# Kernel optimization log

Measured on AMD Instinct MI355X. Metric: run time of the kernel, lower is better.

Reference implementation:

```python
import jax, jax.numpy as jnp
import numpy as np

B, V, H, W = 8, 2, 1024, 1024
N = 131072
TH_MIN, TH_MAX = 0.0, 500.0
ALPHA = 0.5


def _make_extrinsics():
    # Random small-rotation camera-to-world poses (invertible 4x4), fixed seed.
    rng = np.random.default_rng(0)
    E = np.tile(np.eye(4, dtype=np.float32), (B, V, 1, 1))
    for bi in range(B):
        for vi in range(V):
            ang = rng.uniform(-0.15, 0.15)
            ax = rng.normal(size=3)
            ax = ax / np.linalg.norm(ax)
            K = np.array([[0.0, -ax[2], ax[1]], [ax[2], 0.0, -ax[0]], [-ax[1], ax[0], 0.0]])
            R = np.eye(3) + np.sin(ang) * K + (1.0 - np.cos(ang)) * (K @ K)
            E[bi, vi, :3, :3] = R.astype(np.float32)
            E[bi, vi, :3, 3] = (rng.normal(size=3) * 0.5).astype(np.float32)
    return jnp.asarray(E)


def setup_inputs():
    key = jax.random.key(0)
    k0, k1, k2, k3, k4 = jax.random.split(key, 5)
    scale = jnp.array([W - 1.0, H - 1.0], jnp.float32)
    mkpts0 = jax.random.uniform(k0, (N, 2), dtype=jnp.float32) * scale
    mkpts1 = jax.random.uniform(k1, (N, 2), dtype=jnp.float32) * scale
    mconf = jax.random.uniform(k2, (N,), jnp.float32, 0.2, 1.0)
    mbids = jnp.sort(jax.random.randint(k3, (N,), 0, B, dtype=jnp.int32))
    intr = jnp.tile(jnp.array([[1.0, 0.0, 0.5], [0.0, 1.0, 0.5], [0.0, 0.0, 1.0]], jnp.float32), (B, V, 1, 1))
    extr = _make_extrinsics()
    disps = jax.random.uniform(k4, (V * B, 1, H, W), jnp.float32, 0.01, 1.0)
    return {"mkpts0": mkpts0, "mkpts1": mkpts1, "mconf": mconf, "mbids": mbids,
            "intrinsics": intr, "extrinsics": extr, "fullres_disps": disps}


def _forward(mkpts0, mkpts1, mconf, mbids, intrinsics, extrinsics, fullres_disps):
    b, v = intrinsics.shape[:2]
    _, _, h, w = fullres_disps.shape
    # intr0[0,:]*=w ; intr0[1,:]*=h  (normalized -> pixel intrinsics)
    row_scale = jnp.array([float(w), float(h), 1.0], intrinsics.dtype)[None, None, :, None]
    intr = intrinsics * row_scale                                    # (b,v,3,3)
    extr_inv = jnp.linalg.inv(extrinsics)                            # (b,v,4,4)
    proj = jnp.einsum('bvij,bvjk->bvik', intr, extr_inv[:, :, :3, :])  # (b,v,3,4)

    # --- per-keypoint DLT triangulation (vectorized over all N matches) ---
    P = proj[mbids]                                                  # (N,v,3,4)
    pts2 = jnp.stack([mkpts0, mkpts1], axis=1)                       # (N,v,2)
    # rows: conf*(x*P[2]-P[0]), conf*(y*P[2]-P[1])
    A = P[:, :, 2:3, :] * pts2[..., None] - P[:, :, :2, :]           # (N,v,2,4)
    A = A * mconf[:, None, None, None]
    A = A.reshape(-1, 2 * v, 4)                                      # (N,4,4)
    _, _, vh = jnp.linalg.svd(A, full_matrices=False)
    hom = vh[:, -1, :]                                               # last right singular vector
    pts_world = hom[:, :3] / hom[:, 3:4]                             # (N,3)

    # transform into each camera frame: pc_transform(pts, extr.inverse())
    pw_h = jnp.concatenate([pts_world, jnp.ones_like(pts_world[:, :1])], axis=-1)
    pts_cam = jnp.einsum('nvij,nj->nvi', extr_inv[mbids], pw_h)[..., :3]  # (N,v,3)
    z = pts_cam[..., 2]                                              # (N,v)
    valid = jnp.all((z > TH_MIN) & (z < TH_MAX), axis=1)             # (N,)

    # --- near/far over valid matched depths per (scene, view) ---
    zmin = jnp.where(valid[:, None], z, jnp.inf)
    zmax = jnp.where(valid[:, None], z, -jnp.inf)
    near = jax.ops.segment_min(zmin, mbids, num_segments=b)          # (b,v)
    far = jax.ops.segment_max(zmax, mbids, num_segments=b)
    has = jax.ops.segment_max(valid.astype(jnp.float32), mbids, num_segments=b)
    flag = jnp.broadcast_to(has[:, None], (b, v))                    # (b,v)
    near = jnp.where(flag > 0, near, 0.0)
    far = jnp.where(flag > 0, far, 500.0)

    # --- fusion_mkpt_costvolum: scatter 1/z into the cost-volume disparities ---
    disps = fullres_disps.reshape(v, b, h, w)                        # '(v b) 1 h w'
    mk_x = jnp.clip(jnp.stack([mkpts0[:, 0], mkpts1[:, 0]], 1).astype(jnp.int32), 0, w - 1)  # (N,v)
    mk_y = jnp.clip(jnp.stack([mkpts0[:, 1], mkpts1[:, 1]], 1).astype(jnp.int32), 0, h - 1)
    mk_z = 1.0 / z                                                   # matched disparity (N,v)
    view_idx = jnp.broadcast_to(jnp.arange(v, dtype=jnp.int32)[None, :], mk_x.shape)
    bids2 = jnp.broadcast_to(mbids[:, None], mk_x.shape)
    cost = disps[view_idx, bids2, mk_y, mk_x]                        # gather existing disparity
    val = ALPHA * mk_z + (1.0 - ALPHA) * cost                        # alpha-weighted fusion
    val = jnp.where(valid[:, None], val, cost)                       # masked-out matches: no-op write
    disps = disps.at[view_idx, bids2, mk_y, mk_x].set(val)
    fused = disps.reshape(v * b, 1, h, w)
    return fused, near, far, flag


def reference(mkpts0, mkpts1, mconf, mbids, intrinsics, extrinsics, fullres_disps):
    return _forward(mkpts0, mkpts1, mconf, mbids, intrinsics, extrinsics, fullres_disps)
```

## Files before the change

### kernel.cpp

```cpp
#include <hip/hip_runtime.h>
#include <math.h>

#define BB 8
#define VV 2
#define HH 1024
#define WW 1024
#define NPTS 131072
#define IMG (HH*WW)
#define FUSED (VV*BB*IMG)

#define OFF_PD   0u
#define OFF_E2   1536u
#define OFF_HAS  2048u
#define OFF_VAL  2304u
#define OFF_PIX  (2304u + 4u*2u*NPTS)
#define OFF_WIN  (OFF_PIX + 4u*2u*NPTS)
#define WS_NEED  ((size_t)OFF_WIN + 4ull*(size_t)FUSED)

__device__ __forceinline__ int clampi(int v, int lo, int hi) {
    return v < lo ? lo : (v > hi ? hi : v);
}

__global__ __launch_bounds__(64) void prep_kernel(const float* __restrict__ intr,
                            const float* __restrict__ extr,
                            float* __restrict__ out, char* __restrict__ ws) {
    double* Pd  = (double*)(ws + OFF_PD);
    double* e2d = (double*)(ws + OFF_E2);
    int*    hasb = (int*)(ws + OFF_HAS);
    int t = threadIdx.x;
    if (t < BB) hasb[t] = 0;
    if (t < BB * VV) {
        float* near_ = out + FUSED;
        float* far_  = out + FUSED + BB * VV;
        near_[t] = INFINITY;
        far_[t]  = 0.0f;
        const float* E = extr + t * 16;
        double a[4][8];
        for (int i = 0; i < 4; i++)
            for (int j = 0; j < 4; j++) {
                a[i][j]     = (double)E[i * 4 + j];
                a[i][4 + j] = (i == j) ? 1.0 : 0.0;
            }
        for (int c = 0; c < 4; c++) {
            int piv = c; double best = fabs(a[c][c]);
            for (int r = c + 1; r < 4; r++) {
                double v = fabs(a[r][c]);
                if (v > best) { best = v; piv = r; }
            }
            if (piv != c)
                for (int j = 0; j < 8; j++) {
                    double tmp = a[c][j]; a[c][j] = a[piv][j]; a[piv][j] = tmp;
                }
            double inv = 1.0 / a[c][c];
            for (int j = 0; j < 8; j++) a[c][j] *= inv;
            for (int r = 0; r < 4; r++) {
                if (r == c) continue;
                double f = a[r][c];
                for (int j = 0; j < 8; j++) a[r][j] -= f * a[c][j];
            }
        }
        const float* K = intr + t * 9;
        double rs[3] = {(double)WW, (double)HH, 1.0};
        for (int i = 0; i < 3; i++)
            for (int k = 0; k < 4; k++) {
                double s = 0.0;
                for (int j = 0; j < 3; j++) s += (double)K[i * 3 + j] * rs[i] * a[j][4 + k];
                Pd[t * 12 + i * 4 + k] = s;
            }
        for (int k = 0; k < 4; k++) e2d[t * 4 + k] = a[2][4 + k];
    }
}

__global__ __launch_bounds__(256) void copy_kernel(const float4* __restrict__ src,
                                                   float4* __restrict__ dst) {
    int i = blockIdx.x * blockDim.x + threadIdx.x;
    dst[i] = src[i];
}

__global__ __launch_bounds__(256) void clear_kernel(const float* __restrict__ mk0,
                             const float* __restrict__ mk1,
                             const int* __restrict__ mbids, char* __restrict__ ws) {
    int id = blockIdx.x * blockDim.x + threadIdx.x;
    if (id >= 2 * NPTS) return;
    int n = id >> 1, v = id & 1;
    const float* mk = v ? mk1 : mk0;
    int xi = clampi((int)mk[2 * n], 0, WW - 1);
    int yi = clampi((int)mk[2 * n + 1], 0, HH - 1);
    int bid = mbids[n];
    int* winner = (int*)(ws + OFF_WIN);
    winner[(v * BB + bid) * IMG + yi * WW + xi] = -1;
}

template <bool DIRECT>
__global__ __launch_bounds__(256, 2) void solve_kernel(const float* __restrict__ mk0,
                             const float* __restrict__ mk1,
                             const int* __restrict__ mbids, const float* __restrict__ disps,
                             float* __restrict__ out, char* __restrict__ ws) {
    int n = blockIdx.x * blockDim.x + threadIdx.x;
    if (n >= NPTS) return;
    const double* Pd  = (const double*)(ws + OFF_PD);
    const double* e2d = (const double*)(ws + OFF_E2);
    int*   hasb   = (int*)(ws + OFF_HAS);
    float* valarr = (float*)(ws + OFF_VAL);
    int*   pixarr = (int*)(ws + OFF_PIX);
    int*   winner = (int*)(ws + OFF_WIN);
    float* near_  = out + FUSED;
    float* far_   = out + FUSED + BB * VV;

    int bid = mbids[n];
    float xf[2] = {mk0[2 * n], mk1[2 * n]};
    float yf[2] = {mk0[2 * n + 1], mk1[2 * n + 1]};

    double M[4][4];
#pragma unroll
    for (int i = 0; i < 4; i++)
#pragma unroll
        for (int j = 0; j < 4; j++) M[i][j] = 0.0;
#pragma unroll
    for (int v = 0; v < 2; v++) {
        const double* P = Pd + (bid * VV + v) * 12;
        double xx = (double)xf[v], yy = (double)yf[v];
        double r0[4], r1[4];
#pragma unroll
        for (int j = 0; j < 4; j++) {
            r0[j] = xx * P[8 + j] - P[j];
            r1[j] = yy * P[8 + j] - P[4 + j];
        }
#pragma unroll
        for (int i = 0; i < 4; i++)
#pragma unroll
            for (int j = 0; j < 4; j++) M[i][j] += r0[i] * r0[j] + r1[i] * r1[j];
    }

    double Vm[4][4] = {{1, 0, 0, 0}, {0, 1, 0, 0}, {0, 0, 1, 0}, {0, 0, 0, 1}};
    for (int sweep = 0; sweep < 8; ++sweep) {
        double off = fabs(M[0][1]) + fabs(M[0][2]) + fabs(M[0][3]) +
                     fabs(M[1][2]) + fabs(M[1][3]) + fabs(M[2][3]);
        double dia = fabs(M[0][0]) + fabs(M[1][1]) + fabs(M[2][2]) + fabs(M[3][3]);
        if (off <= 1e-13 * dia) break;
#pragma unroll
        for (int p = 0; p < 3; p++) {
#pragma unroll
            for (int q = p + 1; q < 4; q++) {
                double apq = M[p][q];
                if (fabs(apq) < 1e-300) continue;
                double tau = (M[q][q] - M[p][p]) / (2.0 * apq);
                double rt  = sqrt(1.0 + tau * tau);
                double t_  = (tau >= 0.0) ? 1.0 / (tau + rt) : 1.0 / (tau - rt);
                double c = 1.0 / sqrt(1.0 + t_ * t_);
                double s = t_ * c;
#pragma unroll
                for (int k = 0; k < 4; k++) {
                    double mp = M[k][p], mq = M[k][q];
                    M[k][p] = c * mp - s * mq;
                    M[k][q] = s * mp + c * mq;
                }
#pragma unroll
                for (int k = 0; k < 4; k++) {
                    double mp = M[p][k], mq = M[q][k];
                    M[p][k] = c * mp - s * mq;
                    M[q][k] = s * mp + c * mq;
                }
#pragma unroll
                for (int k = 0; k < 4; k++) {
                    double vp = Vm[k][p], vq = Vm[k][q];
                    Vm[k][p] = c * vp - s * vq;
                    Vm[k][q] = s * vp + c * vq;
                }
            }
        }
    }
    int jmin = 0; double dmin = M[0][0];
    if (M[1][1] < dmin) { dmin = M[1][1]; jmin = 1; }
    if (M[2][2] < dmin) { dmin = M[2][2]; jmin = 2; }
    if (M[3][3] < dmin) { dmin = M[3][3]; jmin = 3; }

    double ev[4];
#pragma unroll
    for (int i = 0; i < 4; i++) {
        double a01 = (jmin == 0) ? Vm[i][0] : Vm[i][1];
        double a23 = (jmin == 2) ? Vm[i][2] : Vm[i][3];
        ev[i] = (jmin < 2) ? a01 : a23;
    }

    double iw = 1.0 / ev[3];
    double pwx = ev[0] * iw, pwy = ev[1] * iw, pwz = ev[2] * iw;

    double z[2];
#pragma unroll
    for (int v = 0; v < 2; v++) {
        const double* e = e2d + (bid * VV + v) * 4;
        z[v] = e[0] * pwx + e[1] * pwy + e[2] * pwz + e[3];
    }
    bool valid = (z[0] > 0.0) && (z[0] < 500.0) && (z[1] > 0.0) && (z[1] < 500.0);

    unsigned long long vb = __ballot(valid);
    int bidFirst = __shfl(bid, 0);
    int bidLast  = __shfl(bid, 63);
    if (bidFirst == bidLast) {
        if (vb != 0ULL) {
            float zn[2], zf[2];
#pragma unroll
            for (int v = 0; v < 2; v++) {
                zn[v] = valid ? (float)z[v] : INFINITY;
                zf[v] = valid ? (float)z[v] : -1.0f;
            }
#pragma unroll
            for (int off = 32; off > 0; off >>= 1) {
#pragma unroll
                for (int v = 0; v < 2; v++) {
                    zn[v] = fminf(zn[v], __shfl_down(zn[v], off));
                    zf[v] = fmaxf(zf[v], __shfl_down(zf[v], off));
                }
            }
            if ((threadIdx.x & 63) == 0) {
#pragma unroll
                for (int v = 0; v < 2; v++) {
                    atomicMin((int*)(near_ + bid * VV + v), __float_as_int(zn[v]));
                    atomicMax((int*)(far_  + bid * VV + v), __float_as_int(zf[v]));
                }
                atomicOr(hasb + bid, 1);
            }
        }
    } else if (valid) {
#pragma unroll
        for (int v = 0; v < 2; v++) {
            int fb = __float_as_int((float)z[v]);
            atomicMin((int*)(near_ + bid * VV + v), fb);
            atomicMax((int*)(far_  + bid * VV + v), fb);
        }
        atomicOr(hasb + bid, 1);
    }

#pragma unroll
    for (int v = 0; v < 2; v++) {
        int xi = clampi((int)xf[v], 0, WW - 1);
        int yi = clampi((int)yf[v], 0, HH - 1);
        int pix = (v * BB + bid) * IMG + yi * WW + xi;
        float cost = disps[pix];
        float val = valid ? (float)(0.5 * (1.0 / z[v]) + 0.5 * (double)cost) : cost;
        if (DIRECT) {
            out[pix] = val;
        } else {
            valarr[2 * n + v] = val;
            pixarr[2 * n + v] = pix;
            atomicMax(winner + pix, n);
        }
    }
}

__global__ __launch_bounds__(256) void resolve_kernel(float* __restrict__ out,
                                                      const char* __restrict__ ws) {
    int id = blockIdx.x * blockDim.x + threadIdx.x;
    if (id >= 2 * NPTS) return;
    const float* valarr = (const float*)(ws + OFF_VAL);
    const int*   pixarr = (const int*)(ws + OFF_PIX);
    const int*   winner = (const int*)(ws + OFF_WIN);
    int pix = pixarr[id];
    if (winner[pix] == (id >> 1)) out[pix] = valarr[id];
}

__global__ __launch_bounds__(64) void finalize_kernel(float* __restrict__ out,
                                                      const char* __restrict__ ws) {
    int t = threadIdx.x;
    if (t >= BB * VV) return;
    const int* hasb = (const int*)(ws + OFF_HAS);
    int has = hasb[t / VV];
    float* near_ = out + FUSED;
    float* far_  = out + FUSED + BB * VV;
    float* flag_ = out + FUSED + 2 * BB * VV;
    near_[t] = has ? near_[t] : 0.0f;
    far_[t]  = has ? far_[t]  : 500.0f;
    flag_[t] = has ? 1.0f : 0.0f;
}

extern "C" void kernel_launch(void* const* d_in, const int* in_sizes, int n_in,
                              void* d_out, int out_size, void* d_ws, size_t ws_size,
                              hipStream_t stream) {
    const float* mk0   = (const float*)d_in[0];
    const float* mk1   = (const float*)d_in[1];
    const int*   mbids = (const int*)d_in[3];
    const float* intr  = (const float*)d_in[4];
    const float* extr  = (const float*)d_in[5];
    const float* disps = (const float*)d_in[6];
    float* out = (float*)d_out;
    char*  ws  = (char*)d_ws;

    bool dedup = (ws_size >= WS_NEED);

    prep_kernel<<<1, 64, 0, stream>>>(intr, extr, out, ws);
    copy_kernel<<<FUSED / 4 / 256, 256, 0, stream>>>((const float4*)disps, (float4*)out);
    if (dedup) {
        clear_kernel<<<(2 * NPTS + 255) / 256, 256, 0, stream>>>(mk0, mk1, mbids, ws);
        solve_kernel<false><<<(NPTS + 255) / 256, 256, 0, stream>>>(mk0, mk1, mbids, disps, out, ws);
        resolve_kernel<<<(2 * NPTS + 255) / 256, 256, 0, stream>>>(out, ws);
    } else {
        solve_kernel<true><<<(NPTS + 255) / 256, 256, 0, stream>>>(mk0, mk1, mbids, disps, out, ws);
    }
    finalize_kernel<<<1, 64, 0, stream>>>(out, ws);
}
```

Baseline: 225.9 us.

## Fuse setup kernels, stage projections in LDS, defer disparity gather to resolve

Merges the prep, copy and clear kernels into one launch, and folds finalize into the resolve kernel, cutting the launch count from six to three. The solve kernel now stages the projection and extrinsic rows in shared memory and loads keypoints as float2. It stores z instead of the fused value, so the disparity gather runs only for winning valid matches in resolve. This trades fewer launches and random reads for one more workspace array and branching in the fused kernel.

```diff
diff --git a/kernel.cpp b/kernel.cpp
--- a/kernel.cpp
+++ b/kernel.cpp
@@ -12,104 +12,109 @@
 #define OFF_PD   0u
 #define OFF_E2   1536u
 #define OFF_HAS  2048u
-#define OFF_VAL  2304u
-#define OFF_PIX  (2304u + 4u*2u*NPTS)
-#define OFF_WIN  (OFF_PIX + 4u*2u*NPTS)
+#define OFF_Z    2304u
+#define OFF_PIX  (2304u + 8u*NPTS)
+#define OFF_WIN  (OFF_PIX + 8u*NPTS)
 #define WS_NEED  ((size_t)OFF_WIN + 4ull*(size_t)FUSED)
+
+#define NCOPY  (FUSED/4/256)
+#define NCLEAR ((2*NPTS)/256)
 
 __device__ __forceinline__ int clampi(int v, int lo, int hi) {
     return v < lo ? lo : (v > hi ? hi : v);
 }
 
-__global__ __launch_bounds__(64) void prep_kernel(const float* __restrict__ intr,
-                            const float* __restrict__ extr,
-                            float* __restrict__ out, char* __restrict__ ws) {
-    double* Pd  = (double*)(ws + OFF_PD);
-    double* e2d = (double*)(ws + OFF_E2);
-    int*    hasb = (int*)(ws + OFF_HAS);
+__global__ __launch_bounds__(256) void setup_kernel(
+        const float4* __restrict__ src, float4* __restrict__ dst,
+        const float* __restrict__ mk0, const float* __restrict__ mk1,
+        const int* __restrict__ mbids,
+        const float* __restrict__ intr, const float* __restrict__ extr,
+        float* __restrict__ out, char* __restrict__ ws, int dedup) {
+    int b = blockIdx.x, t = threadIdx.x;
+    if (b < NCOPY) {
+        int i = b * 256 + t;
+        dst[i] = src[i];
+        return;
+    }
+    int cb = b - NCOPY;
+    int id = cb * 256 + t;
+    if (dedup) {
+        int n = id >> 1, v = id & 1;
+        const float* mk = v ? mk1 : mk0;
+        int xi = clampi((int)mk[2 * n], 0, WW - 1);
+        int yi = clampi((int)mk[2 * n + 1], 0, HH - 1);
+        int bid = mbids[n];
+        ((int*)(ws + OFF_WIN))[(v * BB + bid) * IMG + yi * WW + xi] = -1;
+    }
+    if (cb == 0) {
+        if (t < BB) ((int*)(ws + OFF_HAS))[t] = 0;
+        if (t < BB * VV) {
+            float* near_ = out + FUSED;
+            float* far_  = out + FUSED + BB * VV;
+            near_[t] = INFINITY;
+            far_[t]  = 0.0f;
+            double* Pd  = (double*)(ws + OFF_PD);
+            double* e2d = (double*)(ws + OFF_E2);
+            const float* E = extr + t * 16;
+            double a[4][8];
+            for (int i = 0; i < 4; i++)
+                for (int j = 0; j < 4; j++) {
+                    a[i][j]     = (double)E[i * 4 + j];
+                    a[i][4 + j] = (i == j) ? 1.0 : 0.0;
+                }
+            for (int c = 0; c < 4; c++) {
+                int piv = c; double best = fabs(a[c][c]);
+                for (int r = c + 1; r < 4; r++) {
+                    double v = fabs(a[r][c]);
+                    if (v > best) { best = v; piv = r; }
+                }
+                if (piv != c)
+                    for (int j = 0; j < 8; j++) {
+                        double tmp = a[c][j]; a[c][j] = a[piv][j]; a[piv][j] = tmp;
+                    }
+                double inv = 1.0 / a[c][c];
+                for (int j = 0; j < 8; j++) a[c][j] *= inv;
+                for (int r = 0; r < 4; r++) {
+                    if (r == c) continue;
+                    double f = a[r][c];
+                    for (int j = 0; j < 8; j++) a[r][j] -= f * a[c][j];
+                }
+            }
+            const float* K = intr + t * 9;
+            double rs[3] = {(double)WW, (double)HH, 1.0};
+            for (int i = 0; i < 3; i++)
+                for (int k = 0; k < 4; k++) {
+                    double s = 0.0;
+                    for (int j = 0; j < 3; j++) s += (double)K[i * 3 + j] * rs[i] * a[j][4 + k];
+                    Pd[t * 12 + i * 4 + k] = s;
+                }
+            for (int k = 0; k < 4; k++) e2d[t * 4 + k] = a[2][4 + k];
+        }
+    }
+}
+
+template <bool DIRECT>
+__global__ __launch_bounds__(256) void solve_kernel(
+        const float2* __restrict__ mk0, const float2* __restrict__ mk1,
+        const int* __restrict__ mbids, const float* __restrict__ disps,
+        float* __restrict__ out, char* __restrict__ ws) {
+    __shared__ double sD[256];
     int t = threadIdx.x;
-    if (t < BB) hasb[t] = 0;
-    if (t < BB * VV) {
-        float* near_ = out + FUSED;
-        float* far_  = out + FUSED + BB * VV;
-        near_[t] = INFINITY;
-        far_[t]  = 0.0f;
-        const float* E = extr + t * 16;
-        double a[4][8];
-        for (int i = 0; i < 4; i++)
-            for (int j = 0; j < 4; j++) {
-                a[i][j]     = (double)E[i * 4 + j];
-                a[i][4 + j] = (i == j) ? 1.0 : 0.0;
-            }
-        for (int c = 0; c < 4; c++) {
-            int piv = c; double best = fabs(a[c][c]);
-            for (int r = c + 1; r < 4; r++) {
-                double v = fabs(a[r][c]);
-                if (v > best) { best = v; piv = r; }
-            }
-            if (piv != c)
-                for (int j = 0; j < 8; j++) {
-                    double tmp = a[c][j]; a[c][j] = a[piv][j]; a[piv][j] = tmp;
-                }
-            double inv = 1.0 / a[c][c];
-            for (int j = 0; j < 8; j++) a[c][j] *= inv;
-            for (int r = 0; r < 4; r++) {
-                if (r == c) continue;
-                double f = a[r][c];
-                for (int j = 0; j < 8; j++) a[r][j] -= f * a[c][j];
-            }
-        }
-        const float* K = intr + t * 9;
-        double rs[3] = {(double)WW, (double)HH, 1.0};
-        for (int i = 0; i < 3; i++)
-            for (int k = 0; k < 4; k++) {
-                double s = 0.0;
-                for (int j = 0; j < 3; j++) s += (double)K[i * 3 + j] * rs[i] * a[j][4 + k];
-                Pd[t * 12 + i * 4 + k] = s;
-            }
-        for (int k = 0; k < 4; k++) e2d[t * 4 + k] = a[2][4 + k];
-    }
-}
-
-__global__ __launch_bounds__(256) void copy_kernel(const float4* __restrict__ src,
-                                                   float4* __restrict__ dst) {
-    int i = blockIdx.x * blockDim.x + threadIdx.x;
-    dst[i] = src[i];
-}
-
-__global__ __launch_bounds__(256) void clear_kernel(const float* __restrict__ mk0,
-                             const float* __restrict__ mk1,
-                             const int* __restrict__ mbids, char* __restrict__ ws) {
-    int id = blockIdx.x * blockDim.x + threadIdx.x;
-    if (id >= 2 * NPTS) return;
-    int n = id >> 1, v = id & 1;
-    const float* mk = v ? mk1 : mk0;
-    int xi = clampi((int)mk[2 * n], 0, WW - 1);
-    int yi = clampi((int)mk[2 * n + 1], 0, HH - 1);
-    int bid = mbids[n];
-    int* winner = (int*)(ws + OFF_WIN);
-    winner[(v * BB + bid) * IMG + yi * WW + xi] = -1;
-}
-
-template <bool DIRECT>
-__global__ __launch_bounds__(256, 2) void solve_kernel(const float* __restrict__ mk0,
-                             const float* __restrict__ mk1,
-                             const int* __restrict__ mbids, const float* __restrict__ disps,
-                             float* __restrict__ out, char* __restrict__ ws) {
-    int n = blockIdx.x * blockDim.x + threadIdx.x;
-    if (n >= NPTS) return;
-    const double* Pd  = (const double*)(ws + OFF_PD);
-    const double* e2d = (const double*)(ws + OFF_E2);
+    sD[t] = ((const double*)(ws + OFF_PD))[t];
+    __syncthreads();
+
+    int n = blockIdx.x * 256 + t;
     int*   hasb   = (int*)(ws + OFF_HAS);
-    float* valarr = (float*)(ws + OFF_VAL);
+    float* zarr   = (float*)(ws + OFF_Z);
     int*   pixarr = (int*)(ws + OFF_PIX);
     int*   winner = (int*)(ws + OFF_WIN);
     float* near_  = out + FUSED;
     float* far_   = out + FUSED + BB * VV;
 
     int bid = mbids[n];
-    float xf[2] = {mk0[2 * n], mk1[2 * n]};
-    float yf[2] = {mk0[2 * n + 1], mk1[2 * n + 1]};
+    float2 q0 = mk0[n], q1 = mk1[n];
+    float xf[2] = {q0.x, q1.x};
+    float yf[2] = {q0.y, q1.y};
 
     double M[4][4];
 #pragma unroll
@@ -118,7 +123,7 @@
         for (int j = 0; j < 4; j++) M[i][j] = 0.0;
 #pragma unroll
     for (int v = 0; v < 2; v++) {
-        const double* P = Pd + (bid * VV + v) * 12;
+        const double* P = sD + (bid * VV + v) * 12;
         double xx = (double)xf[v], yy = (double)yf[v];
         double r0[4], r1[4];
 #pragma unroll
@@ -183,13 +188,13 @@
         ev[i] = (jmin < 2) ? a01 : a23;
     }
 
-    double iw = 1.0 / ev[3];
+    double iw  = 1.0 / ev[3];
     double pwx = ev[0] * iw, pwy = ev[1] * iw, pwz = ev[2] * iw;
 
     double z[2];
 #pragma unroll
     for (int v = 0; v < 2; v++) {
-        const double* e = e2d + (bid * VV + v) * 4;
+        const double* e = sD + 192 + (bid * VV + v) * 4;
         z[v] = e[0] * pwx + e[1] * pwy + e[2] * pwz + e[3];
     }
     bool valid = (z[0] > 0.0) && (z[0] < 500.0) && (z[1] > 0.0) && (z[1] < 500.0);
@@ -237,27 +242,42 @@
         int xi = clampi((int)xf[v], 0, WW - 1);
         int yi = clampi((int)yf[v], 0, HH - 1);
         int pix = (v * BB + bid) * IMG + yi * WW + xi;
-        float cost = disps[pix];
-        float val = valid ? (float)(0.5 * (1.0 / z[v]) + 0.5 * (double)cost) : cost;
         if (DIRECT) {
+            float cost = disps[pix];
+            float val = valid ? (float)(0.5 * (1.0 / z[v]) + 0.5 * (double)cost) : cost;
             out[pix] = val;
         } else {
-            valarr[2 * n + v] = val;
+            zarr[2 * n + v]   = valid ? (float)z[v] : 0.0f;
             pixarr[2 * n + v] = pix;
             atomicMax(winner + pix, n);
         }
     }
 }
 
-__global__ __launch_bounds__(256) void resolve_kernel(float* __restrict__ out,
+__global__ __launch_bounds__(256) void resolve_kernel(const float* __restrict__ disps,
+                                                      float* __restrict__ out,
                                                       const char* __restrict__ ws) {
-    int id = blockIdx.x * blockDim.x + threadIdx.x;
-    if (id >= 2 * NPTS) return;
-    const float* valarr = (const float*)(ws + OFF_VAL);
+    int id = blockIdx.x * 256 + threadIdx.x;
+    const float* zarr   = (const float*)(ws + OFF_Z);
     const int*   pixarr = (const int*)(ws + OFF_PIX);
     const int*   winner = (const int*)(ws + OFF_WIN);
-    int pix = pixarr[id];
-    if (winner[pix] == (id >> 1)) out[pix] = valarr[id];
+    int   pix = pixarr[id];
+    float zf  = zarr[id];
+    if (winner[pix] == (id >> 1) && zf > 0.0f) {
+        float cost = disps[pix];
+        out[pix] = (float)(0.5 * (1.0 / (double)zf) + 0.5 * (double)cost);
+    }
+    if (blockIdx.x == 0 && threadIdx.x < BB * VV) {
+        int tt = threadIdx.x;
+        const int* hasb = (const int*)(ws + OFF_HAS);
+        int has = hasb[tt / VV];
+        float* near_ = out + FUSED;
+        float* far_  = out + FUSED + BB * VV;
+        float* flag_ = out + FUSED + 2 * BB * VV;
+        near_[tt] = has ? near_[tt] : 0.0f;
+        far_[tt]  = has ? far_[tt]  : 500.0f;
+        flag_[tt] = has ? 1.0f : 0.0f;
+    }
 }
 
 __global__ __launch_bounds__(64) void finalize_kernel(float* __restrict__ out,
@@ -288,14 +308,16 @@
 
     bool dedup = (ws_size >= WS_NEED);
 
-    prep_kernel<<<1, 64, 0, stream>>>(intr, extr, out, ws);
-    copy_kernel<<<FUSED / 4 / 256, 256, 0, stream>>>((const float4*)disps, (float4*)out);
+    setup_kernel<<<NCOPY + NCLEAR, 256, 0, stream>>>(
+        (const float4*)disps, (float4*)out, mk0, mk1, mbids, intr, extr, out, ws,
+        dedup ? 1 : 0);
     if (dedup) {
-        clear_kernel<<<(2 * NPTS + 255) / 256, 256, 0, stream>>>(mk0, mk1, mbids, ws);
-        solve_kernel<false><<<(NPTS + 255) / 256, 256, 0, stream>>>(mk0, mk1, mbids, disps, out, ws);
-        resolve_kernel<<<(2 * NPTS + 255) / 256, 256, 0, stream>>>(out, ws);
+        solve_kernel<false><<<NPTS / 256, 256, 0, stream>>>(
+            (const float2*)mk0, (const float2*)mk1, mbids, disps, out, ws);
+        resolve_kernel<<<NCLEAR, 256, 0, stream>>>(disps, out, ws);
     } else {
-        solve_kernel<true><<<(NPTS + 255) / 256, 256, 0, stream>>>(mk0, mk1, mbids, disps, out, ws);
-    }
-    finalize_kernel<<<1, 64, 0, stream>>>(out, ws);
-}
+        solve_kernel<true><<<NPTS / 256, 256, 0, stream>>>(
+            (const float2*)mk0, (const float2*)mk1, mbids, disps, out, ws);
+        finalize_kernel<<<1, 64, 0, stream>>>(out, ws);
+    }
+}
```

New measurement: 214.9 us. 4.9% less time.
